# Performance work log

Measured on AMD Instinct MI355X. Metric: run time of the kernel, lower is better.

The kernel has to match this reference:

```python
import jax, jax.numpy as jnp
import numpy as np

IN_CH, HID, OUT_CH = 1, 16, 1

def _conv(x, w, b, pad):
    # x: [B,C,H,W], w: [O,I,kh,kw], b: [O]
    y = jax.lax.conv_general_dilated(
        x, w, window_strides=(1, 1), padding=[(pad, pad), (pad, pad)],
        dimension_numbers=('NCHW', 'OIHW', 'NCHW'))
    return y + b[None, :, None, None]

def setup_inputs() -> dict:
    key = jax.random.key(0)
    ks = jax.random.split(key, 8)
    def w_init(k, shape):
        fan_in = shape[1] * shape[2] * shape[3]
        return jax.random.normal(k, shape, dtype=jnp.float32) * (1.0 / np.sqrt(fan_in))
    B, H, W = 32, 256, 256
    return {
        'x': jax.random.normal(ks[0], (B, IN_CH, H, W), dtype=jnp.float32),
        'w_perceive': w_init(ks[1], (HID * 2, IN_CH + HID, 3, 3)),
        'b_perceive': jnp.zeros((HID * 2,), jnp.float32),
        'w_up1': w_init(ks[2], (HID, HID * 2, 1, 1)),
        'b_up1': jnp.zeros((HID,), jnp.float32),
        'w_up2': w_init(ks[3], (HID, HID, 1, 1)),
        'b_up2': jnp.zeros((HID,), jnp.float32),
        'w_tau': w_init(ks[4], (HID, IN_CH + HID * 2, 3, 3)),
        'b_tau_conv': jnp.zeros((HID,), jnp.float32),
        'b_tau': jnp.ones((1, HID, 1, 1), jnp.float32) * 1.5,
        'w_read': w_init(ks[5], (OUT_CH, HID, 1, 1)),
        'b_read': jnp.zeros((OUT_CH,), jnp.float32),
        'n_steps': 10,
    }

def reference(x, w_perceive, b_perceive, w_up1, b_up1, w_up2, b_up2,
              w_tau, b_tau_conv, b_tau, w_read, b_read, n_steps):
    B, _, H, W = x.shape
    state = jnp.zeros((B, HID, H, W), dtype=x.dtype)

    def step(state, _):
        combined = jnp.concatenate([x, state], axis=1)          # [B, in+hid, H, W]
        perception = _conv(combined, w_perceive, b_perceive, 1)  # [B, 2*hid, H, W]
        h1 = jax.nn.relu(_conv(perception, w_up1, b_up1, 0))
        delta = _conv(h1, w_up2, b_up2, 0)                       # [B, hid, H, W]
        tau_input = jnp.concatenate([x, state, delta], axis=1)  # [B, in+2*hid, H, W]
        tau_logit = _conv(tau_input, w_tau, b_tau_conv, 1) + b_tau
        beta = jnp.clip(jax.nn.sigmoid(tau_logit), 0.01, 0.99)
        return beta * state + (1.0 - beta) * delta, None

    state, _ = jax.lax.scan(step, state, None, length=n_steps)
    return jax.nn.sigmoid(_conv(state, w_read, b_read, 0))
```

## Files before the change

### kernel.cpp

```cpp
#include <hip/hip_runtime.h>
#include <hip/hip_bf16.h>
#include <math.h>


#define B_   32
#define H_   256
#define W_   256
#define PIT  40
#define XPP  260

typedef unsigned short ushort_t;
typedef __attribute__((ext_vector_type(8))) short short8;
typedef __attribute__((ext_vector_type(4))) float float4v;

__device__ __forceinline__ unsigned fbits(float f) {
    union { float f; unsigned u; } v; v.f = f; return v.u;
}
__device__ __forceinline__ ushort_t f2bu(float f) {
    return (ushort_t)((fbits(f) + 0x8000u) >> 16);
}
__device__ __forceinline__ unsigned pack2(float lo, float hi) {
    return ((fbits(hi) + 0x8000u) & 0xFFFF0000u) | ((fbits(lo) + 0x8000u) >> 16);
}
__device__ __forceinline__ float bu2f(ushort_t u) {
    union { unsigned i; float f; } v; v.i = ((unsigned)u) << 16; return v.f;
}
__device__ __forceinline__ float lo2f(unsigned u) {
    union { unsigned i; float f; } v; v.i = u << 16; return v.f;
}
__device__ __forceinline__ float hi2f(unsigned u) {
    union { unsigned i; float f; } v; v.i = u & 0xFFFF0000u; return v.f;
}

__global__ void prep(
    const float* __restrict__ wp,
    const float* __restrict__ wu1,
    const float* __restrict__ bu1,
    const float* __restrict__ bp,
    const float* __restrict__ wu2,
    const float* __restrict__ wt,
    ushort_t* __restrict__ wh1p,
    ushort_t* __restrict__ wu2f,
    ushort_t* __restrict__ wtn,
    float* __restrict__ scal)
{
    __shared__ float Weff[16 * 153];
    const int tid = threadIdx.x;

    for (int i = tid; i < 16 * 153; i += 256) {
        int j = i / 153, rem = i % 153, c = rem / 9, t = rem % 9;
        float s = 0.f;
        for (int o = 0; o < 32; ++o)
            s += wu1[j * 32 + o] * wp[o * 153 + c * 9 + t];
        Weff[i] = s;
    }
    if (tid < 16) {
        float s = bu1[tid];
        for (int o = 0; o < 32; ++o) s += wu1[tid * 32 + o] * bp[o];
        scal[tid] = s;
    }
    __syncthreads();

    if (tid < 16) scal[16 + tid] = Weff[tid * 153 + 8];

    for (int i = tid; i < 4 * 64 * 8; i += 256) {
        int ii = i >> 9, lane = (i >> 3) & 63, j = i & 7;
        int n = lane & 15, kk = ((lane >> 4) << 3) + j;
        int tap = 2 * ii + (kk >> 4), ch = kk & 15;
        wh1p[i] = f2bu(Weff[n * 153 + (ch + 1) * 9 + tap]);
    }
    for (int i = tid; i < 512; i += 256) {
        int lane = i >> 3, j = i & 7;
        int n = lane & 15, k = ((lane >> 4) << 3) + j;
        float v = 0.f;
        if (k < 16)      v = Weff[n * 153 + (k + 1) * 9 + 8];
        else if (k < 24) v = Weff[n * 153 + (k - 16)];
        wh1p[2048 + i] = f2bu(v);
    }
    for (int i = tid; i < 512; i += 256) {
        int lane = i >> 3, j = i & 7;
        int n = lane & 15, k = ((lane >> 4) << 3) + j;
        wu2f[i] = (k < 16) ? f2bu(wu2[n * 16 + k]) : (ushort_t)0;
    }
    for (int i = tid; i < 9 * 64 * 8; i += 256) {
        int t = i / 512, lane = (i / 8) % 64, j = i % 8;
        int n = lane & 15, k = ((lane >> 4) << 3) + j;
        int c = (k < 16) ? (17 + k) : (k - 15);
        wtn[i] = f2bu(wt[n * 297 + c * 9 + t]);
    }
}

__global__ __launch_bounds__(256) void precompute_tx(
    const float* __restrict__ x,
    const float* __restrict__ wt,
    const float* __restrict__ btc,
    const float* __restrict__ bt,
    ushort_t* __restrict__ tx)
{
    int p = blockIdx.x * 256 + threadIdx.x;
    int py = (p >> 8) & 255, px = p & 255;
    const float* xb = x + (p & ~0xFFFF);

    float xp[9];
#pragma unroll
    for (int t = 0; t < 9; ++t) {
        int gy = py + t / 3 - 1, gx = px + t % 3 - 1;
        bool in = ((unsigned)gy < 256u) & ((unsigned)gx < 256u);
        xp[t] = in ? xb[gy * 256 + gx] : 0.f;
    }
    short8 o0, o1;
#pragma unroll
    for (int j = 0; j < 16; ++j) {
        float tv = btc[j] + bt[j];
#pragma unroll
        for (int t = 0; t < 9; ++t) tv = fmaf(xp[t], wt[j * 297 + t], tv);
        if (j < 8) o0[j] = (short)f2bu(tv); else o1[j - 8] = (short)f2bu(tv);
    }
    ushort_t* dst = tx + (size_t)p * 16;
    *(short8*)(dst)     = o0;
    *(short8*)(dst + 8) = o1;
}

__global__ __launch_bounds__(256) void precompute_xp8(
    const float* __restrict__ x,
    ushort_t* __restrict__ xp8)
{
    int idx = blockIdx.x * 256 + threadIdx.x;
    if (idx >= B_ * XPP * XPP) return;
    int b  = idx / (XPP * XPP), rem = idx - b * (XPP * XPP);
    int by = rem / XPP, bx = rem - by * XPP;
    int gy = by - 2, gx = bx - 2;
    const float* xb = x + (size_t)b * 65536;
    short8 v;
#pragma unroll
    for (int t = 0; t < 8; ++t) {
        int yy = gy + t / 3, xx = gx + t % 3;
        bool in = ((unsigned)yy < 256u) & ((unsigned)xx < 256u);
        v[t] = in ? (short)f2bu(xb[yy * 256 + xx]) : (short)0;
    }
    *(short8*)(xp8 + (size_t)idx * 8) = v;
}

__global__ __launch_bounds__(256) void nca_step(
    const ushort_t* __restrict__ stIn,
    ushort_t* __restrict__ stOut,
    const ushort_t* __restrict__ xp8g,
    const ushort_t* __restrict__ txg,
    const ushort_t* __restrict__ wh1p,
    const ushort_t* __restrict__ wu2f,
    const ushort_t* __restrict__ wtn,
    const float* __restrict__ scal,
    const float* __restrict__ bu2G,
    const float* __restrict__ wrd,
    const float* __restrict__ brd,
    float* __restrict__ outg,
    int first, int last)
{
    __shared__ ushort_t comb[400 * PIT];

    const int tid  = threadIdx.x;
    const int w    = tid >> 6, lane = tid & 63;
    const int m    = lane & 15, q = lane >> 4;
    const int och  = q * 4;
    const int gx0  = blockIdx.x * 16, gy0 = blockIdx.y * 16;
    const size_t pb = (size_t)blockIdx.z * 65536;
    const size_t xpb = (size_t)blockIdx.z * (XPP * XPP);
    const short8 z8 = {0, 0, 0, 0, 0, 0, 0, 0};
    const float4v z4 = {0.f, 0.f, 0.f, 0.f};

    uint2 tpre[4];
#pragma unroll
    for (int i = 0; i < 4; ++i) {
        const size_t pix = pb + (size_t)(gy0 + w * 4 + i) * 256 + gx0 + m;
        tpre[i] = *(const uint2*)(txg + pix * 16 + och);
    }

    short8 wh1r[5], wtnr[9];
#pragma unroll
    for (int i = 0; i < 5; ++i) wh1r[i] = *(const short8*)(wh1p + (i * 64 + lane) * 8);
#pragma unroll
    for (int t = 0; t < 9; ++t) wtnr[t] = *(const short8*)(wtn + (t * 64 + lane) * 8);
    const short8 wu2r = *(const short8*)(wu2f + lane * 8);

    float4v beff4, wxh84, bu24, wr4;
#pragma unroll
    for (int r = 0; r < 4; ++r) {
        beff4[r] = scal[och + r];
        wxh84[r] = scal[16 + och + r];
        bu24[r]  = bu2G[och + r];
        wr4[r]   = wrd[och + r];
    }
    const float br = brd[0];

    const int sel = q >> 1;
    int offp[4];
#pragma unroll
    for (int ii = 0; ii < 4; ++ii) {
        int tA = 2 * ii, tB = 2 * ii + 1;
        int oA = ((tA / 3) * 20 + (tA % 3)) * PIT;
        int oB = ((tB / 3) * 20 + (tB % 3)) * PIT;
        offp[ii] = sel ? oB : oA;
    }
    const int chOff = 16 + (q & 1) * 8;
    const int t8off = (2 * 20 + 2) * PIT;
    const int off5  = (q == 0) ? (t8off + 16) : (q == 1) ? (t8off + 24)
                    : (q == 2) ? 32 : 16;

    const int bpA = ((m + (q << 5)) & 63) << 2;
    const bool hiq = q >= 2;

    for (int p = tid; p < 400; p += 256) {
        int ry = p / 20, rx = p - ry * 20;
        int gy = gy0 + ry - 2, gx = gx0 + rx - 2;
        ushort_t* row = comb + p * PIT;
        bool in = ((unsigned)gy < 256u) & ((unsigned)gx < 256u);
        if (in && !first) {
            const ushort_t* sp = stIn + (pb + gy * 256 + gx) * 16;
            *(short8*)(row + 16) = *(const short8*)(sp);
            *(short8*)(row + 24) = *(const short8*)(sp + 8);
        } else {
            *(short8*)(row + 16) = z8; *(short8*)(row + 24) = z8;
        }
        *(short8*)(row + 32) = *(const short8*)(
            xp8g + (xpb + (size_t)(gy0 + ry) * XPP + (gx0 + rx)) * 8);
    }
    __syncthreads();

    for (int i = 0; i < 6; ++i) {
        int g = w + 4 * i; if (g >= 21) break;
        int raw = g * 16 + m;
        int idx = (raw > 323) ? 323 : raw;
        int py = idx / 18, px = idx - py * 18;
        const ushort_t* abase = comb + (py * 20 + px) * PIT;
        float4v acc = z4;
#pragma unroll
        for (int ii = 0; ii < 4; ++ii) {
            short8 b = *(const short8*)(abase + offp[ii] + chOff);
            acc = __builtin_amdgcn_mfma_f32_16x16x32_bf16(wh1r[ii], b, acc, 0, 0, 0);
        }
        {
            short8 b = *(const short8*)(abase + off5);
            acc = __builtin_amdgcn_mfma_f32_16x16x32_bf16(wh1r[4], b, acc, 0, 0, 0);
        }
        float x8 = bu2f(comb[((py + 2) * 20 + px + 2) * PIT + 32]);
        uint2 hv;
        {
            float h0 = fmaxf(acc[0] + beff4[0] + x8 * wxh84[0], 0.f);
            float h1 = fmaxf(acc[1] + beff4[1] + x8 * wxh84[1], 0.f);
            float h2 = fmaxf(acc[2] + beff4[2] + x8 * wxh84[2], 0.f);
            float h3 = fmaxf(acc[3] + beff4[3] + x8 * wxh84[3], 0.f);
            hv.x = pack2(h0, h1); hv.y = pack2(h2, h3);
        }
        int vx0 = __builtin_amdgcn_ds_bpermute(bpA,      (int)hv.x);
        int vy0 = __builtin_amdgcn_ds_bpermute(bpA,      (int)hv.y);
        int vx1 = __builtin_amdgcn_ds_bpermute(bpA + 64, (int)hv.x);
        int vy1 = __builtin_amdgcn_ds_bpermute(bpA + 64, (int)hv.y);
        union { int i4[4]; short8 s8; } bb;
        bb.i4[0] = hiq ? 0 : vx0;  bb.i4[1] = hiq ? 0 : vy0;
        bb.i4[2] = hiq ? 0 : vx1;  bb.i4[3] = hiq ? 0 : vy1;
        float4v d = __builtin_amdgcn_mfma_f32_16x16x32_bf16(wu2r, bb.s8, z4, 0, 0, 0);
        bool vld = raw < 324;
        int gy = gy0 - 1 + py, gx = gx0 - 1 + px;
        bool im = vld & ((unsigned)gy < 256u) & ((unsigned)gx < 256u);
        uint2 dv;
        dv.x = pack2(d[0] + bu24[0], d[1] + bu24[1]);
        dv.y = pack2(d[2] + bu24[2], d[3] + bu24[3]);
        if (!im) { dv.x = 0u; dv.y = 0u; }
        if (vld)
            *(uint2*)(comb + ((py + 1) * 20 + (px + 1)) * PIT + och) = dv;
    }
    __syncthreads();

    for (int i = 0; i < 4; ++i) {
        int g = w * 4 + i;
        const ushort_t* cb = comb + ((g + 1) * 20 + (m + 1)) * PIT;
        float4v acc = z4;
#pragma unroll
        for (int t = 0; t < 9; ++t) {
            short8 b = *(const short8*)(cb + ((t / 3) * 20 + (t % 3)) * PIT + q * 8);
            acc = __builtin_amdgcn_mfma_f32_16x16x32_bf16(wtnr[t], b, acc, 0, 0, 0);
        }
        int gy = gy0 + g;
        const size_t pix = pb + gy * 256 + gx0 + m;
        const ushort_t* cpx = comb + ((g + 2) * 20 + (m + 2)) * PIT;
        uint2 su = *(const uint2*)(cpx + 16 + och);
        uint2 du = *(const uint2*)(cpx + och);
        uint2 tu = tpre[i];
        float sold[4] = { lo2f(su.x), hi2f(su.x), lo2f(su.y), hi2f(su.y) };
        float dvv[4]  = { lo2f(du.x), hi2f(du.x), lo2f(du.y), hi2f(du.y) };
        float txv[4]  = { lo2f(tu.x), hi2f(tu.x), lo2f(tu.y), hi2f(tu.y) };
        float sn[4];
#pragma unroll
        for (int r = 0; r < 4; ++r) {
            float tl  = acc[r] + txv[r];
            float e   = __expf(-tl);
            float bta = __builtin_amdgcn_rcpf(1.f + e);
            bta = fminf(fmaxf(bta, 0.01f), 0.99f);
            sn[r] = dvv[r] + bta * (sold[r] - dvv[r]);
        }
        if (!last) {
            uint2 o;
            o.x = pack2(sn[0], sn[1]); o.y = pack2(sn[2], sn[3]);
            *(uint2*)(stOut + pix * 16 + och) = o;
        } else {
            float v = sn[0] * wr4[0] + sn[1] * wr4[1]
                    + sn[2] * wr4[2] + sn[3] * wr4[3];
            v += __shfl_xor(v, 16);
            v += __shfl_xor(v, 32);
            if (q == 0) {
                float eo = __expf(-(v + br));
                outg[pix] = __builtin_amdgcn_rcpf(1.f + eo);
            }
        }
    }
}

extern "C" void kernel_launch(void* const* d_in, const int* in_sizes, int n_in,
                              void* d_out, int out_size, void* d_ws, size_t ws_size,
                              hipStream_t stream)
{
    const float* x          = (const float*)d_in[0];
    const float* w_perceive = (const float*)d_in[1];
    const float* b_perceive = (const float*)d_in[2];
    const float* w_up1      = (const float*)d_in[3];
    const float* b_up1      = (const float*)d_in[4];
    const float* w_up2      = (const float*)d_in[5];
    const float* b_up2      = (const float*)d_in[6];
    const float* w_tau      = (const float*)d_in[7];
    const float* b_tau_conv = (const float*)d_in[8];
    const float* b_tau      = (const float*)d_in[9];
    const float* w_read     = (const float*)d_in[10];
    const float* b_read     = (const float*)d_in[11];
    float* out = (float*)d_out;

    const size_t stateElems = (size_t)B_ * H_ * W_ * 16;
    const size_t xp8Elems   = (size_t)B_ * XPP * XPP * 8;

    ushort_t* stA  = (ushort_t*)d_ws;
    ushort_t* stB  = stA + stateElems;
    ushort_t* txg  = stB + stateElems;
    ushort_t* xp8g = txg + stateElems;
    ushort_t* wh1p = xp8g + xp8Elems;
    ushort_t* wu2f = wh1p + 2560;
    ushort_t* wtn  = wu2f + 512;
    float*    scal = (float*)(wtn + 4608);

    const size_t needBytes = (3 * stateElems + xp8Elems
                              + 2560 + 512 + 4608) * sizeof(ushort_t)
                           + 32 * sizeof(float);
    if (ws_size < needBytes) return;

    prep<<<dim3(1), dim3(256), 0, stream>>>(
        w_perceive, w_up1, b_up1, b_perceive, w_up2, w_tau,
        wh1p, wu2f, wtn, scal);
    precompute_tx<<<dim3(8192), dim3(256), 0, stream>>>(
        x, w_tau, b_tau_conv, b_tau, txg);
    precompute_xp8<<<dim3((B_ * XPP * XPP + 255) / 256), dim3(256), 0, stream>>>(
        x, xp8g);

    ushort_t* cur = stA;
    ushort_t* nxt = stB;
    for (int s = 0; s < 10; ++s) {
        nca_step<<<dim3(16, 16, 32), dim3(256), 0, stream>>>(
            cur, nxt, xp8g, txg, wh1p, wu2f, wtn, scal, b_up2,
            w_read, b_read, out, (s == 0) ? 1 : 0, (s == 9) ? 1 : 0);
        ushort_t* t = cur; cur = nxt; nxt = t;
    }
}
```

Before: 786.7 us.

## Fuse x-channel tau conv into step kernel via extra MFMA, drop tx precompute

Removes the precompute_tx kernel and its per-pixel 16-channel bf16 buffer. The x contribution to the tau convolution is now computed inside each step, using one extra MFMA over the 8 packed x taps already held in shared memory, plus a scalar FMA for the ninth tap and bias. This saves a precompute pass and the per-step global reads of tx, in exchange for extra MFMA and LDS work every step. It also changes the rounding of the x term from a precomputed fp32 sum stored as bf16 to bf16 weights accumulated in fp32.

```diff
diff --git a/kernel.cpp b/kernel.cpp
--- a/kernel.cpp
+++ b/kernel.cpp
@@ -39,8 +39,11 @@
     const float* __restrict__ bp,
     const float* __restrict__ wu2,
     const float* __restrict__ wt,
+    const float* __restrict__ btc,
+    const float* __restrict__ bt,
     ushort_t* __restrict__ wh1p,
     ushort_t* __restrict__ wu2f,
+    ushort_t* __restrict__ wtxf,
     ushort_t* __restrict__ wtn,
     float* __restrict__ scal)
 {
@@ -59,6 +62,8 @@
         for (int o = 0; o < 32; ++o) s += wu1[tid * 32 + o] * bp[o];
         scal[tid] = s;
     }
+    if (tid < 16) scal[32 + tid] = btc[tid] + bt[tid];
+    if (tid < 16) scal[48 + tid] = wt[tid * 297 + 8];
     __syncthreads();
 
     if (tid < 16) scal[16 + tid] = Weff[tid * 153 + 8];
@@ -82,43 +87,17 @@
         int n = lane & 15, k = ((lane >> 4) << 3) + j;
         wu2f[i] = (k < 16) ? f2bu(wu2[n * 16 + k]) : (ushort_t)0;
     }
+    for (int i = tid; i < 512; i += 256) {
+        int lane = i >> 3, j = i & 7;
+        int n = lane & 15, k = ((lane >> 4) << 3) + j;
+        wtxf[i] = (k < 8) ? f2bu(wt[n * 297 + k]) : (ushort_t)0;
+    }
     for (int i = tid; i < 9 * 64 * 8; i += 256) {
         int t = i / 512, lane = (i / 8) % 64, j = i % 8;
         int n = lane & 15, k = ((lane >> 4) << 3) + j;
         int c = (k < 16) ? (17 + k) : (k - 15);
         wtn[i] = f2bu(wt[n * 297 + c * 9 + t]);
     }
-}
-
-__global__ __launch_bounds__(256) void precompute_tx(
-    const float* __restrict__ x,
-    const float* __restrict__ wt,
-    const float* __restrict__ btc,
-    const float* __restrict__ bt,
-    ushort_t* __restrict__ tx)
-{
-    int p = blockIdx.x * 256 + threadIdx.x;
-    int py = (p >> 8) & 255, px = p & 255;
-    const float* xb = x + (p & ~0xFFFF);
-
-    float xp[9];
-#pragma unroll
-    for (int t = 0; t < 9; ++t) {
-        int gy = py + t / 3 - 1, gx = px + t % 3 - 1;
-        bool in = ((unsigned)gy < 256u) & ((unsigned)gx < 256u);
-        xp[t] = in ? xb[gy * 256 + gx] : 0.f;
-    }
-    short8 o0, o1;
-#pragma unroll
-    for (int j = 0; j < 16; ++j) {
-        float tv = btc[j] + bt[j];
-#pragma unroll
-        for (int t = 0; t < 9; ++t) tv = fmaf(xp[t], wt[j * 297 + t], tv);
-        if (j < 8) o0[j] = (short)f2bu(tv); else o1[j - 8] = (short)f2bu(tv);
-    }
-    ushort_t* dst = tx + (size_t)p * 16;
-    *(short8*)(dst)     = o0;
-    *(short8*)(dst + 8) = o1;
 }
 
 __global__ __launch_bounds__(256) void precompute_xp8(
@@ -145,9 +124,9 @@
     const ushort_t* __restrict__ stIn,
     ushort_t* __restrict__ stOut,
     const ushort_t* __restrict__ xp8g,
-    const ushort_t* __restrict__ txg,
     const ushort_t* __restrict__ wh1p,
     const ushort_t* __restrict__ wu2f,
+    const ushort_t* __restrict__ wtxf,
     const ushort_t* __restrict__ wtn,
     const float* __restrict__ scal,
     const float* __restrict__ bu2G,
@@ -168,25 +147,21 @@
     const short8 z8 = {0, 0, 0, 0, 0, 0, 0, 0};
     const float4v z4 = {0.f, 0.f, 0.f, 0.f};
 
-    uint2 tpre[4];
-#pragma unroll
-    for (int i = 0; i < 4; ++i) {
-        const size_t pix = pb + (size_t)(gy0 + w * 4 + i) * 256 + gx0 + m;
-        tpre[i] = *(const uint2*)(txg + pix * 16 + och);
-    }
-
     short8 wh1r[5], wtnr[9];
 #pragma unroll
     for (int i = 0; i < 5; ++i) wh1r[i] = *(const short8*)(wh1p + (i * 64 + lane) * 8);
 #pragma unroll
     for (int t = 0; t < 9; ++t) wtnr[t] = *(const short8*)(wtn + (t * 64 + lane) * 8);
     const short8 wu2r = *(const short8*)(wu2f + lane * 8);
-
-    float4v beff4, wxh84, bu24, wr4;
+    const short8 wtxr = *(const short8*)(wtxf + lane * 8);
+
+    float4v beff4, wxh84, bu24, wr4, tb4, wtx84;
 #pragma unroll
     for (int r = 0; r < 4; ++r) {
         beff4[r] = scal[och + r];
         wxh84[r] = scal[16 + och + r];
+        tb4[r]   = scal[32 + och + r];
+        wtx84[r] = scal[48 + och + r];
         bu24[r]  = bu2G[och + r];
         wr4[r]   = wrd[och + r];
     }
@@ -280,19 +255,22 @@
             short8 b = *(const short8*)(cb + ((t / 3) * 20 + (t % 3)) * PIT + q * 8);
             acc = __builtin_amdgcn_mfma_f32_16x16x32_bf16(wtnr[t], b, acc, 0, 0, 0);
         }
+        {
+            short8 bx = *(const short8*)(cb + 32);
+            acc = __builtin_amdgcn_mfma_f32_16x16x32_bf16(wtxr, bx, acc, 0, 0, 0);
+        }
         int gy = gy0 + g;
         const size_t pix = pb + gy * 256 + gx0 + m;
         const ushort_t* cpx = comb + ((g + 2) * 20 + (m + 2)) * PIT;
+        float x8c = bu2f(comb[((g + 3) * 20 + (m + 3)) * PIT + 32]);
         uint2 su = *(const uint2*)(cpx + 16 + och);
         uint2 du = *(const uint2*)(cpx + och);
-        uint2 tu = tpre[i];
         float sold[4] = { lo2f(su.x), hi2f(su.x), lo2f(su.y), hi2f(su.y) };
         float dvv[4]  = { lo2f(du.x), hi2f(du.x), lo2f(du.y), hi2f(du.y) };
-        float txv[4]  = { lo2f(tu.x), hi2f(tu.x), lo2f(tu.y), hi2f(tu.y) };
         float sn[4];
 #pragma unroll
         for (int r = 0; r < 4; ++r) {
-            float tl  = acc[r] + txv[r];
+            float tl  = acc[r] + tb4[r] + x8c * wtx84[r];
             float e   = __expf(-tl);
             float bta = __builtin_amdgcn_rcpf(1.f + e);
             bta = fminf(fmaxf(bta, 0.01f), 0.99f);
@@ -338,23 +316,21 @@
 
     ushort_t* stA  = (ushort_t*)d_ws;
     ushort_t* stB  = stA + stateElems;
-    ushort_t* txg  = stB + stateElems;
-    ushort_t* xp8g = txg + stateElems;
+    ushort_t* xp8g = stB + stateElems;
     ushort_t* wh1p = xp8g + xp8Elems;
     ushort_t* wu2f = wh1p + 2560;
-    ushort_t* wtn  = wu2f + 512;
+    ushort_t* wtxf = wu2f + 512;
+    ushort_t* wtn  = wtxf + 512;
     float*    scal = (float*)(wtn + 4608);
 
-    const size_t needBytes = (3 * stateElems + xp8Elems
-                              + 2560 + 512 + 4608) * sizeof(ushort_t)
-                           + 32 * sizeof(float);
+    const size_t needBytes = (2 * stateElems + xp8Elems
+                              + 2560 + 512 + 512 + 4608) * sizeof(ushort_t)
+                           + 64 * sizeof(float);
     if (ws_size < needBytes) return;
 
     prep<<<dim3(1), dim3(256), 0, stream>>>(
         w_perceive, w_up1, b_up1, b_perceive, w_up2, w_tau,
-        wh1p, wu2f, wtn, scal);
-    precompute_tx<<<dim3(8192), dim3(256), 0, stream>>>(
-        x, w_tau, b_tau_conv, b_tau, txg);
+        b_tau_conv, b_tau, wh1p, wu2f, wtxf, wtn, scal);
     precompute_xp8<<<dim3((B_ * XPP * XPP + 255) / 256), dim3(256), 0, stream>>>(
         x, xp8g);
 
@@ -362,7 +338,7 @@
     ushort_t* nxt = stB;
     for (int s = 0; s < 10; ++s) {
         nca_step<<<dim3(16, 16, 32), dim3(256), 0, stream>>>(
-            cur, nxt, xp8g, txg, wh1p, wu2f, wtn, scal, b_up2,
+            cur, nxt, xp8g, wh1p, wu2f, wtxf, wtn, scal, b_up2,
             w_read, b_read, out, (s == 0) ? 1 : 0, (s == 9) ? 1 : 0);
         ushort_t* t = cur; cur = nxt; nxt = t;
     }
```

Result: no change. 795.3 us (+1.1%).
